# Optimization experiments

Measured on AMD Instinct MI355X. Metric: run time of the kernel, lower is better.

The kernel has to match this reference:

```python
import jax, jax.numpy as jnp
import numpy as np

VOXEL_SIZE = 0.05  # from init_kwargs


def _voxel_ds(pts, voxel_size, key, L):
    """Voxel-grid downsample one cloud (N,3): mean of points per occupied voxel,
    then resample L voxel centroids (uniform with replacement among valid voxels).
    Static shapes throughout (jit/vmap friendly)."""
    N = pts.shape[0]
    mn = jnp.min(pts, axis=0)
    v = jnp.floor((pts - mn) / voxel_size).astype(jnp.int32)      # (N,3) voxel coords >= 0
    dims = jnp.max(v, axis=0) + 1                                  # traced grid extents
    lin = (v[:, 0] * dims[1] + v[:, 1]) * dims[2] + v[:, 2]        # linearized voxel id
    order = jnp.argsort(lin)
    sl = lin[order]
    is_new = jnp.concatenate([jnp.ones((1,), bool), sl[1:] != sl[:-1]])
    seg = jnp.cumsum(is_new) - 1                                   # compact segment id per sorted point
    num_vox = seg[-1] + 1                                          # traced count of occupied voxels
    sums = jax.ops.segment_sum(pts[order], seg, num_segments=N)    # (N,3) padded
    cnt = jax.ops.segment_sum(jnp.ones((N,), pts.dtype), seg, num_segments=N)
    means = sums / jnp.maximum(cnt, 1.0)[:, None]                  # voxel centroids
    # random resample L centroids among the first num_vox valid segments
    u = jax.random.uniform(key, (L,))
    idx = jnp.minimum((u * num_vox.astype(u.dtype)).astype(jnp.int32), num_vox - 1)
    return means[idx]                                              # (L,3)


def _voxel_layer(x, voxel_size, L, key):
    # x: (B,3,N) -> (B,3,L)
    B = x.shape[0]
    pts = jnp.transpose(x, (0, 2, 1))                              # (B,N,3)
    keys = jax.random.split(key, B)
    out = jax.vmap(lambda p, k: _voxel_ds(p, voxel_size, k, L))(pts, keys)
    return jnp.transpose(out, (0, 2, 1))                           # (B,3,L)


def setup_inputs() -> dict:
    key = jax.random.key(0)
    x = jax.random.uniform(key, (16, 3, 262144), dtype=jnp.float32)
    return {"x": x}


def reference(x):
    B, _, N = x.shape
    L1, L2 = N // 2, N // 4
    k1, k2 = jax.random.split(jax.random.key(42))
    voxel_x1 = _voxel_layer(x, VOXEL_SIZE, L1, k1)
    voxel_x2 = _voxel_layer(voxel_x1, 2.0 * VOXEL_SIZE, L2, k2)
    return (voxel_x1, voxel_x2)
```

## Files before the change

kernel.cpp:

```cpp
#include <hip/hip_runtime.h>
#include <stdint.h>


typedef unsigned int u32;
typedef unsigned long long u64;

struct KeyArr { uint32_t k0[16]; uint32_t k1[16]; };

__host__ __device__ inline void tf2x32(uint32_t k0, uint32_t k1,
                                       uint32_t c0, uint32_t c1,
                                       uint32_t& o0, uint32_t& o1) {
  const uint32_t ks0 = k0, ks1 = k1, ks2 = k0 ^ k1 ^ 0x1BD11BDAu;
  uint32_t x0 = c0 + ks0, x1 = c1 + ks1;
#define TF_R(r) { x0 += x1; x1 = (x1 << (r)) | (x1 >> (32 - (r))); x1 ^= x0; }
  TF_R(13) TF_R(15) TF_R(26) TF_R(6)
  x0 += ks1; x1 += ks2 + 1u;
  TF_R(17) TF_R(29) TF_R(16) TF_R(24)
  x0 += ks2; x1 += ks0 + 2u;
  TF_R(13) TF_R(15) TF_R(26) TF_R(6)
  x0 += ks0; x1 += ks1 + 3u;
  TF_R(17) TF_R(29) TF_R(16) TF_R(24)
  x0 += ks1; x1 += ks2 + 4u;
  TF_R(13) TF_R(15) TF_R(26) TF_R(6)
  x0 += ks2; x1 += ks0 + 5u;
#undef TF_R
  o0 = x0; o1 = x1;
}

#define MN1 262144
#define ML1 131072
#define ML2 65536
#define MG1 8000
#define MG2 1000

__device__ __forceinline__ void bin1(float px, float py, float pz, float m0,
                                     float m1, float m2, float vox, int S,
                                     u64* lA, u64* lB) {
  int v0 = (int)floorf((px - m0) / vox);
  int v1 = (int)floorf((py - m1) / vox);
  int v2 = (int)floorf((pz - m2) / vox);
  int lin = (v0 * S + v1) * S + v2;
  u32 qx = (u32)(px * 1048576.0f);
  u32 qy = (u32)(py * 1048576.0f);
  u32 qz = (u32)(pz * 1048576.0f);
  atomicAdd(&lA[lin], ((u64)qy << 32) | (u64)qx);
  atomicAdd(&lB[lin], (1ull << 32) | (u64)qz);
}

__global__ void init_kernel(u64* cellsA, u64* cellsB, int ncells) {
  int i = blockIdx.x * blockDim.x + threadIdx.x;
  int stride = gridDim.x * blockDim.x;
  for (int j = i; j < ncells; j += stride) { cellsA[j] = 0ull; cellsB[j] = 0ull; }
}

__global__ void min_kernel(const float* __restrict__ in, int n4,
                           float* __restrict__ pmin) {
  int row = blockIdx.y;
  int PB = gridDim.x;
  const float4* p = (const float4*)in + (size_t)row * n4;
  int base = blockIdx.x * 2048 + threadIdx.x;
  float4 v0 = p[base], v1 = p[base + 256], v2 = p[base + 512],
         v3 = p[base + 768], v4 = p[base + 1024], v5 = p[base + 1280],
         v6 = p[base + 1536], v7 = p[base + 1792];
  float m0 = fminf(fminf(v0.x, v0.y), fminf(v0.z, v0.w));
  float m1 = fminf(fminf(v1.x, v1.y), fminf(v1.z, v1.w));
  float m2 = fminf(fminf(v2.x, v2.y), fminf(v2.z, v2.w));
  float m3 = fminf(fminf(v3.x, v3.y), fminf(v3.z, v3.w));
  float m4 = fminf(fminf(v4.x, v4.y), fminf(v4.z, v4.w));
  float m5 = fminf(fminf(v5.x, v5.y), fminf(v5.z, v5.w));
  float m6 = fminf(fminf(v6.x, v6.y), fminf(v6.z, v6.w));
  float m7 = fminf(fminf(v7.x, v7.y), fminf(v7.z, v7.w));
  float m = fminf(fminf(fminf(m0, m1), fminf(m2, m3)),
                  fminf(fminf(m4, m5), fminf(m6, m7)));
  for (int off = 32; off > 0; off >>= 1)
    m = fminf(m, __shfl_down(m, off, 64));
  __shared__ float wmin[4];
  int wid = threadIdx.x >> 6;
  if ((threadIdx.x & 63) == 0) wmin[wid] = m;
  __syncthreads();
  if (threadIdx.x == 0)
    pmin[row * PB + blockIdx.x] =
        fminf(fminf(wmin[0], wmin[1]), fminf(wmin[2], wmin[3]));
}

template <int G, int S, bool ATOMIC>
__global__ __launch_bounds__(1024) void accum_kernel(
    const float* __restrict__ in, int N, float vox,
    const float* __restrict__ pmin, int PB, u64* __restrict__ Ap,
    u64* __restrict__ Bp) {
  extern __shared__ u64 lds[];
  u64* lA = lds;
  u64* lB = lds + G;
  __shared__ float s_m[3];
  int tid = threadIdx.x, b = blockIdx.y;
  for (int i = tid; i < G; i += 1024) { lA[i] = 0ull; lB[i] = 0ull; }
  int wid = tid >> 6, lane = tid & 63;
  if (wid < 3) {
    float v = __int_as_float(0x7F800000);
    for (int j = lane; j < PB; j += 64)
      v = fminf(v, pmin[(b * 3 + wid) * PB + j]);
    for (int off = 32; off > 0; off >>= 1)
      v = fminf(v, __shfl_down(v, off, 64));
    if (lane == 0) s_m[wid] = v;
  }
  __syncthreads();
  float m0 = s_m[0], m1 = s_m[1], m2 = s_m[2];
  int ppb = N / gridDim.x;
  const float* base = in + (size_t)b * 3 * N;
  int start = blockIdx.x * ppb;
  const float4* r0 = (const float4*)(base + start);
  const float4* r1 = (const float4*)(base + N + start);
  const float4* r2 = (const float4*)(base + 2 * N + start);
  int q4 = ppb >> 2;
  for (int i = tid; i < q4; i += 1024) {
    float4 X = r0[i], Y = r1[i], Z = r2[i];
    bin1(X.x, Y.x, Z.x, m0, m1, m2, vox, S, lA, lB);
    bin1(X.y, Y.y, Z.y, m0, m1, m2, vox, S, lA, lB);
    bin1(X.z, Y.z, Z.z, m0, m1, m2, vox, S, lA, lB);
    bin1(X.w, Y.w, Z.w, m0, m1, m2, vox, S, lA, lB);
  }
  __syncthreads();
  int p = ATOMIC ? 0 : blockIdx.x;
  u64* gA = Ap + ((size_t)p * 16 + b) * G;
  u64* gB = Bp + ((size_t)p * 16 + b) * G;
  for (int c = tid; c < G; c += 1024) {
    if (ATOMIC) {
      u64 Bv = lB[c];
      if (Bv) { atomicAdd(&gA[c], lA[c]); atomicAdd(&gB[c], Bv); }
    } else {
      gA[c] = lA[c];
      gB[c] = lB[c];
    }
  }
}

__global__ __launch_bounds__(512) void redcomp1_kernel(
    const u64* __restrict__ Ap, const u64* __restrict__ Bp,
    float4* __restrict__ mc1 , u32* __restrict__ ccnt1) {
  int c = blockIdx.x, b = blockIdx.y;
  int tid = threadIdx.x, lane = tid & 63, wid = tid >> 6;
  __shared__ u32 s_w[16];
  float4 v = make_float4(0.f, 0.f, 0.f, 0.f);
  bool occ = false;
  if (tid < 500) {
    int cell = c * 500 + tid;
    u64 A = 0ull, Bv = 0ull;
#pragma unroll
    for (int p = 0; p < 16; ++p) {
      size_t o = ((size_t)p * 16 + b) * MG1 + cell;
      A += Ap[o];
      Bv += Bp[o];
    }
    u32 cnt = (u32)(Bv >> 32);
    if (cnt) {
      double inv = 1.0 / (1048576.0 * (double)cnt);
      v.x = (float)((double)(u32)A * inv);
      v.y = (float)((double)(u32)(A >> 32) * inv);
      v.z = (float)((double)(u32)Bv * inv);
      occ = true;
    }
  }
  u64 mask = __ballot(occ);
  u32 wpre = (u32)__popcll(mask & ((1ull << lane) - 1ull));
  if (lane == 0) s_w[wid] = (u32)__popcll(mask);
  __syncthreads();
  if (tid == 0) {
    u32 s = 0;
    for (int w = 0; w < 8; ++w) { u32 t = s_w[w]; s_w[8 + w] = s; s += t; }
    ccnt1[b * 16 + c] = s;
  }
  __syncthreads();
  if (occ) mc1[((size_t)b * 16 + c) * 500 + s_w[8 + wid] + wpre] = v;
}

__global__ void sample1_kernel(const float4* __restrict__ mc1,
                               const u32* __restrict__ ccnt1, KeyArr keys,
                               float* __restrict__ out,
                               float* __restrict__ pmin2) {
  int t = blockIdx.x * 256 + threadIdx.x;
  int b = blockIdx.y;
  int l0 = t * 4;
  u32 pre[17];
  pre[0] = 0u;
#pragma unroll
  for (int j = 0; j < 16; ++j) pre[j + 1] = pre[j] + ccnt1[b * 16 + j];
  u32 nv = pre[16];
  float fnv = (float)nv;
  int nvm1 = (int)nv - 1;
  uint32_t K0 = keys.k0[b], K1 = keys.k1[b];
  float4 m[4];
#pragma unroll
  for (int j = 0; j < 4; ++j) {
    uint32_t w0, w1;
    tf2x32(K0, K1, 0u, (uint32_t)(l0 + j), w0, w1);
    uint32_t bits = w0 ^ w1;
    float u = __uint_as_float((bits >> 9) | 0x3F800000u) - 1.0f;
    int idx = (int)(u * fnv);
    if (idx > nvm1) idx = nvm1;
    int ch = 0;
    u32 base = 0u;
#pragma unroll
    for (int q = 1; q < 16; ++q) {
      u32 pq = pre[q];
      if ((u32)idx >= pq) { ch = q; base = pq; }
    }
    m[j] = mc1[((size_t)b * 16 + ch) * 500 + (idx - (int)base)];
  }
  *(float4*)(out + ((size_t)b * 3 + 0) * ML1 + l0) =
      make_float4(m[0].x, m[1].x, m[2].x, m[3].x);
  *(float4*)(out + ((size_t)b * 3 + 1) * ML1 + l0) =
      make_float4(m[0].y, m[1].y, m[2].y, m[3].y);
  *(float4*)(out + ((size_t)b * 3 + 2) * ML1 + l0) =
      make_float4(m[0].z, m[1].z, m[2].z, m[3].z);
  float ax = fminf(fminf(m[0].x, m[1].x), fminf(m[2].x, m[3].x));
  float ay = fminf(fminf(m[0].y, m[1].y), fminf(m[2].y, m[3].y));
  float az = fminf(fminf(m[0].z, m[1].z), fminf(m[2].z, m[3].z));
  for (int off = 32; off > 0; off >>= 1) {
    ax = fminf(ax, __shfl_down(ax, off, 64));
    ay = fminf(ay, __shfl_down(ay, off, 64));
    az = fminf(az, __shfl_down(az, off, 64));
  }
  __shared__ float wm[4][3];
  int wid = threadIdx.x >> 6;
  if ((threadIdx.x & 63) == 0) {
    wm[wid][0] = ax; wm[wid][1] = ay; wm[wid][2] = az;
  }
  __syncthreads();
  if (threadIdx.x == 0) {
    int PB = gridDim.x;
    pmin2[(b * 3 + 0) * PB + blockIdx.x] =
        fminf(fminf(wm[0][0], wm[1][0]), fminf(wm[2][0], wm[3][0]));
    pmin2[(b * 3 + 1) * PB + blockIdx.x] =
        fminf(fminf(wm[0][1], wm[1][1]), fminf(wm[2][1], wm[3][1]));
    pmin2[(b * 3 + 2) * PB + blockIdx.x] =
        fminf(fminf(wm[0][2], wm[1][2]), fminf(wm[2][2], wm[3][2]));
  }
}

template <int G>
__global__ __launch_bounds__(1024) void redcomp_kernel(
    int P, const u64* __restrict__ Ap, const u64* __restrict__ Bp,
    float4* __restrict__ means4, u32* __restrict__ numvox) {
  int b = blockIdx.x, tid = threadIdx.x, wid = tid >> 6, lane = tid & 63;
  u64 A = 0ull, Bv = 0ull;
  if (tid < G) {
    for (int p = 0; p < P; ++p) {
      size_t o = ((size_t)p * 16 + b) * G + tid;
      A += Ap[o];
      Bv += Bp[o];
    }
  }
  u32 cnt = (u32)(Bv >> 32);
  float4 v = make_float4(0.f, 0.f, 0.f, 0.f);
  if (cnt) {
    double inv = 1.0 / (1048576.0 * (double)cnt);
    v.x = (float)((double)(u32)A * inv);
    v.y = (float)((double)(u32)(A >> 32) * inv);
    v.z = (float)((double)(u32)Bv * inv);
  }
  bool occ = cnt > 0u;
  u64 mask = __ballot(occ);
  u32 prefix = (u32)__popcll(mask & ((1ull << lane) - 1ull));
  __shared__ u32 wtot[16], wbase[16];
  if (lane == 0) wtot[wid] = (u32)__popcll(mask);
  __syncthreads();
  if (tid == 0) {
    u32 s = 0;
    for (int w = 0; w < 16; ++w) { wbase[w] = s; s += wtot[w]; }
    numvox[b] = s;
  }
  __syncthreads();
  if (occ) means4[(size_t)b * G + wbase[wid] + prefix] = v;
}

template <bool DOMIN>
__global__ void sample_kernel(int L, int G, const float4* __restrict__ means4,
                              const u32* __restrict__ numvox, KeyArr keys,
                              float* __restrict__ out,
                              float* __restrict__ pmin) {
  int t = blockIdx.x * 256 + threadIdx.x;
  int b = blockIdx.y;
  int l0 = t * 4;
  u32 nv = numvox[b];
  float fnv = (float)nv;
  int nvm1 = (int)nv - 1;
  uint32_t K0 = keys.k0[b], K1 = keys.k1[b];
  float4 m[4];
#pragma unroll
  for (int j = 0; j < 4; ++j) {
    uint32_t w0, w1;
    tf2x32(K0, K1, 0u, (uint32_t)(l0 + j), w0, w1);
    uint32_t bits = w0 ^ w1;
    float u = __uint_as_float((bits >> 9) | 0x3F800000u) - 1.0f;
    int idx = (int)(u * fnv);
    if (idx > nvm1) idx = nvm1;
    m[j] = means4[(size_t)b * G + idx];
  }
  *(float4*)(out + ((size_t)b * 3 + 0) * L + l0) =
      make_float4(m[0].x, m[1].x, m[2].x, m[3].x);
  *(float4*)(out + ((size_t)b * 3 + 1) * L + l0) =
      make_float4(m[0].y, m[1].y, m[2].y, m[3].y);
  *(float4*)(out + ((size_t)b * 3 + 2) * L + l0) =
      make_float4(m[0].z, m[1].z, m[2].z, m[3].z);
  if (DOMIN) {
    float ax = fminf(fminf(m[0].x, m[1].x), fminf(m[2].x, m[3].x));
    float ay = fminf(fminf(m[0].y, m[1].y), fminf(m[2].y, m[3].y));
    float az = fminf(fminf(m[0].z, m[1].z), fminf(m[2].z, m[3].z));
    for (int off = 32; off > 0; off >>= 1) {
      ax = fminf(ax, __shfl_down(ax, off, 64));
      ay = fminf(ay, __shfl_down(ay, off, 64));
      az = fminf(az, __shfl_down(az, off, 64));
    }
    __shared__ float wm[4][3];
    int wid = threadIdx.x >> 6;
    if ((threadIdx.x & 63) == 0) {
      wm[wid][0] = ax; wm[wid][1] = ay; wm[wid][2] = az;
    }
    __syncthreads();
    if (threadIdx.x == 0) {
      int PB = gridDim.x;
      pmin[(b * 3 + 0) * PB + blockIdx.x] =
          fminf(fminf(wm[0][0], wm[1][0]), fminf(wm[2][0], wm[3][0]));
      pmin[(b * 3 + 1) * PB + blockIdx.x] =
          fminf(fminf(wm[0][1], wm[1][1]), fminf(wm[2][1], wm[3][1]));
      pmin[(b * 3 + 2) * PB + blockIdx.x] =
          fminf(fminf(wm[0][2], wm[1][2]), fminf(wm[2][2], wm[3][2]));
    }
  }
}

__global__ __launch_bounds__(1024) void compact_kernel(
    int G, const u64* __restrict__ Ac, const u64* __restrict__ Bc,
    float4* __restrict__ means4, u32* __restrict__ numvox) {
  int b = blockIdx.x, tid = threadIdx.x, wid = tid >> 6, lane = tid & 63;
  __shared__ u32 wtot[16], wbase[16];
  __shared__ u32 gbase;
  if (tid == 0) gbase = 0u;
  __syncthreads();
  for (int t0 = 0; t0 < G; t0 += 1024) {
    int cell = t0 + tid;
    float4 v = make_float4(0.f, 0.f, 0.f, 0.f);
    u32 cnt = 0u;
    if (cell < G) {
      u64 A = Ac[(size_t)b * G + cell], Bv = Bc[(size_t)b * G + cell];
      cnt = (u32)(Bv >> 32);
      if (cnt) {
        double inv = 1.0 / (1048576.0 * (double)cnt);
        v.x = (float)((double)(u32)A * inv);
        v.y = (float)((double)(u32)(A >> 32) * inv);
        v.z = (float)((double)(u32)Bv * inv);
      }
    }
    bool occ = cnt > 0u;
    u64 mask = __ballot(occ);
    u32 prefix = (u32)__popcll(mask & ((1ull << lane) - 1ull));
    if (lane == 0) wtot[wid] = (u32)__popcll(mask);
    __syncthreads();
    if (tid == 0) {
      u32 s = gbase;
      for (int w = 0; w < 16; ++w) { wbase[w] = s; s += wtot[w]; }
      gbase = s;
    }
    __syncthreads();
    if (occ) means4[(size_t)b * G + wbase[wid] + prefix] = v;
    __syncthreads();
  }
  if (tid == 0) numvox[b] = gbase;
}

extern "C" void kernel_launch(void* const* d_in, const int* in_sizes, int n_in,
                              void* d_out, int out_size, void* d_ws,
                              size_t ws_size, hipStream_t stream) {
  const float* x = (const float*)d_in[0];
  float* out = (float*)d_out;

  uint32_t k1a, k1b, k2a, k2b;
  tf2x32(0u, 42u, 0u, 0u, k1a, k1b);
  tf2x32(0u, 42u, 0u, 1u, k2a, k2b);
  KeyArr keys1, keys2;
  for (int b = 0; b < 16; ++b) {
    tf2x32(k1a, k1b, 0u, (uint32_t)b, keys1.k0[b], keys1.k1[b]);
    tf2x32(k2a, k2b, 0u, (uint32_t)b, keys2.k0[b], keys2.k1[b]);
  }

  const int PB1 = 32, PB2 = 128;
  const size_t oAp = 0;
  const size_t oBp = oAp + (size_t)16 * 16 * MG1 * 8;
  const size_t oMc1 = oBp + (size_t)16 * 16 * MG1 * 8;
  const size_t oMc2 = oMc1 + (size_t)16 * 16 * 500 * 16;
  const size_t oPm1 = oMc2 + (size_t)16 * MG2 * 16;
  const size_t oPm2 = oPm1 + 48 * PB1 * 4;
  const size_t oCc1 = oPm2 + 48 * PB2 * 4;
  const size_t oNv = oCc1 + 256 * 4;
  const size_t bigNeed = oNv + 128;

  uint8_t* w = (uint8_t*)d_ws;
  if (ws_size >= bigNeed) {
    u64* Ap = (u64*)(w + oAp);
    u64* Bp = (u64*)(w + oBp);
    float4* mc1 = (float4*)(w + oMc1);
    float4* mc2 = (float4*)(w + oMc2);
    float* pmin1 = (float*)(w + oPm1);
    float* pmin2 = (float*)(w + oPm2);
    u32* ccnt1 = (u32*)(w + oCc1);
    u32* numvox2 = (u32*)(w + oNv);

    min_kernel<<<dim3(PB1, 48), dim3(256), 0, stream>>>(x, MN1 / 4, pmin1);
    accum_kernel<MG1, 20, false>
        <<<dim3(16, 16), dim3(1024), 2 * MG1 * 8, stream>>>(x, MN1, 0.05f,
                                                            pmin1, PB1, Ap, Bp);
    redcomp1_kernel<<<dim3(16, 16), dim3(512), 0, stream>>>(Ap, Bp, mc1,
                                                            ccnt1);
    sample1_kernel<<<dim3(ML1 / 1024, 16), dim3(256), 0, stream>>>(
        mc1, ccnt1, keys1, out, pmin2);
    float* out2 = out + (size_t)48 * ML1;
    accum_kernel<MG2, 10, false>
        <<<dim3(16, 16), dim3(1024), 2 * MG2 * 8, stream>>>(
            out, ML1, 0.1f, pmin2, PB2, Ap, Bp);
    redcomp_kernel<MG2><<<dim3(16), dim3(1024), 0, stream>>>(16, Ap, Bp, mc2,
                                                             numvox2);
    sample_kernel<false><<<dim3(ML2 / 1024, 16), dim3(256), 0, stream>>>(
        ML2, MG2, mc2, numvox2, keys2, out2, nullptr);
    return;
  }

  const size_t slice1 = (size_t)16 * MG1, slice2 = (size_t)16 * MG2;
  u64* As = (u64*)w;
  u64* Bs = As + (slice1 + slice2);
  float4* means4s = (float4*)(Bs + (slice1 + slice2));
  float* pmin1s = (float*)(means4s + slice1);
  float* pmin2s = pmin1s + 48 * PB1;
  u32* numvoxs = (u32*)(pmin2s + 48 * PB2);

  init_kernel<<<dim3(64), dim3(256), 0, stream>>>(As, Bs,
                                                  (int)(slice1 + slice2));
  min_kernel<<<dim3(PB1, 48), dim3(256), 0, stream>>>(x, MN1 / 4, pmin1s);
  accum_kernel<MG1, 20, true>
      <<<dim3(8, 16), dim3(1024), 2 * MG1 * 8, stream>>>(x, MN1, 0.05f, pmin1s,
                                                         PB1, As, Bs);
  compact_kernel<<<dim3(16), dim3(1024), 0, stream>>>(MG1, As, Bs, means4s,
                                                      numvoxs);
  sample_kernel<true><<<dim3(ML1 / 1024, 16), dim3(256), 0, stream>>>(
      ML1, MG1, means4s, numvoxs, keys1, out, pmin2s);
  float* out2 = out + (size_t)48 * ML1;
  accum_kernel<MG2, 10, true>
      <<<dim3(8, 16), dim3(1024), 2 * MG2 * 8, stream>>>(
          out, ML1, 0.1f, pmin2s, PB2, As + slice1, Bs + slice1);
  compact_kernel<<<dim3(16), dim3(1024), 0, stream>>>(
      MG2, As + slice1, Bs + slice1, means4s, numvoxs + 16);
  sample_kernel<false><<<dim3(ML2 / 1024, 16), dim3(256), 0, stream>>>(
      ML2, MG2, means4s, numvoxs + 16, keys2, out2, nullptr);
}
```

Before: 68.76 us.

## Interleave partial accumulators and fuse stage-two reduce, compact and sample

Partial voxel sums are now stored as interleaved (A,B) pairs in one ulonglong2 buffer, so each reducer does a single 16-byte load per partition instead of two separate 8-byte loads. For the second stage, the separate reduce/compact kernel and the sampling kernel are merged into one kernel. Each block reduces the partitions into shared memory, compacts the occupied voxels, and samples from LDS. This removes one launch and a global round-trip for the means, at the cost of every block redundantly repeating the per-batch reduction.

```diff
diff --git a/kernel.cpp b/kernel.cpp
--- a/kernel.cpp
+++ b/kernel.cpp
@@ -83,8 +83,214 @@
         fminf(fminf(wmin[0], wmin[1]), fminf(wmin[2], wmin[3]));
 }
 
-template <int G, int S, bool ATOMIC>
-__global__ __launch_bounds__(1024) void accum_kernel(
+template <int G, int S>
+__global__ __launch_bounds__(1024) void accum_part_kernel(
+    const float* __restrict__ in, int N, float vox,
+    const float* __restrict__ pmin, int PB, ulonglong2* __restrict__ Cp) {
+  extern __shared__ u64 lds[];
+  u64* lA = lds;
+  u64* lB = lds + G;
+  __shared__ float s_m[3];
+  int tid = threadIdx.x, b = blockIdx.y;
+  for (int i = tid; i < G; i += 1024) { lA[i] = 0ull; lB[i] = 0ull; }
+  int wid = tid >> 6, lane = tid & 63;
+  if (wid < 3) {
+    float v = __int_as_float(0x7F800000);
+    for (int j = lane; j < PB; j += 64)
+      v = fminf(v, pmin[(b * 3 + wid) * PB + j]);
+    for (int off = 32; off > 0; off >>= 1)
+      v = fminf(v, __shfl_down(v, off, 64));
+    if (lane == 0) s_m[wid] = v;
+  }
+  __syncthreads();
+  float m0 = s_m[0], m1 = s_m[1], m2 = s_m[2];
+  int ppb = N / gridDim.x;
+  const float* base = in + (size_t)b * 3 * N;
+  int start = blockIdx.x * ppb;
+  const float4* r0 = (const float4*)(base + start);
+  const float4* r1 = (const float4*)(base + N + start);
+  const float4* r2 = (const float4*)(base + 2 * N + start);
+  int q4 = ppb >> 2;
+  for (int i = tid; i < q4; i += 1024) {
+    float4 X = r0[i], Y = r1[i], Z = r2[i];
+    bin1(X.x, Y.x, Z.x, m0, m1, m2, vox, S, lA, lB);
+    bin1(X.y, Y.y, Z.y, m0, m1, m2, vox, S, lA, lB);
+    bin1(X.z, Y.z, Z.z, m0, m1, m2, vox, S, lA, lB);
+    bin1(X.w, Y.w, Z.w, m0, m1, m2, vox, S, lA, lB);
+  }
+  __syncthreads();
+  ulonglong2* gC = Cp + ((size_t)blockIdx.x * 16 + b) * G;
+  for (int c = tid; c < G; c += 1024)
+    gC[c] = make_ulonglong2(lA[c], lB[c]);
+}
+
+__global__ __launch_bounds__(512) void redcomp1_kernel(
+    const ulonglong2* __restrict__ Cp,
+    float4* __restrict__ mc1 , u32* __restrict__ ccnt1) {
+  int c = blockIdx.x, b = blockIdx.y;
+  int tid = threadIdx.x, lane = tid & 63, wid = tid >> 6;
+  __shared__ u32 s_w[16];
+  float4 v = make_float4(0.f, 0.f, 0.f, 0.f);
+  bool occ = false;
+  if (tid < 500) {
+    int cell = c * 500 + tid;
+    u64 A = 0ull, Bv = 0ull;
+#pragma unroll
+    for (int p = 0; p < 16; ++p) {
+      ulonglong2 cc = Cp[((size_t)p * 16 + b) * MG1 + cell];
+      A += cc.x;
+      Bv += cc.y;
+    }
+    u32 cnt = (u32)(Bv >> 32);
+    if (cnt) {
+      double inv = 1.0 / (1048576.0 * (double)cnt);
+      v.x = (float)((double)(u32)A * inv);
+      v.y = (float)((double)(u32)(A >> 32) * inv);
+      v.z = (float)((double)(u32)Bv * inv);
+      occ = true;
+    }
+  }
+  u64 mask = __ballot(occ);
+  u32 wpre = (u32)__popcll(mask & ((1ull << lane) - 1ull));
+  if (lane == 0) s_w[wid] = (u32)__popcll(mask);
+  __syncthreads();
+  if (tid == 0) {
+    u32 s = 0;
+    for (int w = 0; w < 8; ++w) { u32 t = s_w[w]; s_w[8 + w] = s; s += t; }
+    ccnt1[b * 16 + c] = s;
+  }
+  __syncthreads();
+  if (occ) mc1[((size_t)b * 16 + c) * 500 + s_w[8 + wid] + wpre] = v;
+}
+
+__global__ void sample1_kernel(const float4* __restrict__ mc1,
+                               const u32* __restrict__ ccnt1, KeyArr keys,
+                               float* __restrict__ out,
+                               float* __restrict__ pmin2) {
+  int t = blockIdx.x * 256 + threadIdx.x;
+  int b = blockIdx.y;
+  int l0 = t * 4;
+  u32 pre[17];
+  pre[0] = 0u;
+#pragma unroll
+  for (int j = 0; j < 16; ++j) pre[j + 1] = pre[j] + ccnt1[b * 16 + j];
+  u32 nv = pre[16];
+  float fnv = (float)nv;
+  int nvm1 = (int)nv - 1;
+  uint32_t K0 = keys.k0[b], K1 = keys.k1[b];
+  float4 m[4];
+#pragma unroll
+  for (int j = 0; j < 4; ++j) {
+    uint32_t w0, w1;
+    tf2x32(K0, K1, 0u, (uint32_t)(l0 + j), w0, w1);
+    uint32_t bits = w0 ^ w1;
+    float u = __uint_as_float((bits >> 9) | 0x3F800000u) - 1.0f;
+    int idx = (int)(u * fnv);
+    if (idx > nvm1) idx = nvm1;
+    int ch = 0;
+    u32 base = 0u;
+#pragma unroll
+    for (int q = 1; q < 16; ++q) {
+      u32 pq = pre[q];
+      if ((u32)idx >= pq) { ch = q; base = pq; }
+    }
+    m[j] = mc1[((size_t)b * 16 + ch) * 500 + (idx - (int)base)];
+  }
+  *(float4*)(out + ((size_t)b * 3 + 0) * ML1 + l0) =
+      make_float4(m[0].x, m[1].x, m[2].x, m[3].x);
+  *(float4*)(out + ((size_t)b * 3 + 1) * ML1 + l0) =
+      make_float4(m[0].y, m[1].y, m[2].y, m[3].y);
+  *(float4*)(out + ((size_t)b * 3 + 2) * ML1 + l0) =
+      make_float4(m[0].z, m[1].z, m[2].z, m[3].z);
+  float ax = fminf(fminf(m[0].x, m[1].x), fminf(m[2].x, m[3].x));
+  float ay = fminf(fminf(m[0].y, m[1].y), fminf(m[2].y, m[3].y));
+  float az = fminf(fminf(m[0].z, m[1].z), fminf(m[2].z, m[3].z));
+  for (int off = 32; off > 0; off >>= 1) {
+    ax = fminf(ax, __shfl_down(ax, off, 64));
+    ay = fminf(ay, __shfl_down(ay, off, 64));
+    az = fminf(az, __shfl_down(az, off, 64));
+  }
+  __shared__ float wm[4][3];
+  int wid = threadIdx.x >> 6;
+  if ((threadIdx.x & 63) == 0) {
+    wm[wid][0] = ax; wm[wid][1] = ay; wm[wid][2] = az;
+  }
+  __syncthreads();
+  if (threadIdx.x == 0) {
+    int PB = gridDim.x;
+    pmin2[(b * 3 + 0) * PB + blockIdx.x] =
+        fminf(fminf(wm[0][0], wm[1][0]), fminf(wm[2][0], wm[3][0]));
+    pmin2[(b * 3 + 1) * PB + blockIdx.x] =
+        fminf(fminf(wm[0][1], wm[1][1]), fminf(wm[2][1], wm[3][1]));
+    pmin2[(b * 3 + 2) * PB + blockIdx.x] =
+        fminf(fminf(wm[0][2], wm[1][2]), fminf(wm[2][2], wm[3][2]));
+  }
+}
+
+__global__ __launch_bounds__(1024) void sampred2_kernel(
+    const ulonglong2* __restrict__ Cp, KeyArr keys, float* __restrict__ out2) {
+  int g = blockIdx.x, b = blockIdx.y;
+  int tid = threadIdx.x, lane = tid & 63, wid = tid >> 6;
+  __shared__ float4 smeans[MG2];
+  __shared__ u32 s_w[32];
+  __shared__ u32 s_nv;
+  float4 v = make_float4(0.f, 0.f, 0.f, 0.f);
+  bool occ = false;
+  if (tid < MG2) {
+    u64 A = 0ull, Bv = 0ull;
+#pragma unroll
+    for (int p = 0; p < 16; ++p) {
+      ulonglong2 cc = Cp[((size_t)p * 16 + b) * MG2 + tid];
+      A += cc.x;
+      Bv += cc.y;
+    }
+    u32 cnt = (u32)(Bv >> 32);
+    if (cnt) {
+      double inv = 1.0 / (1048576.0 * (double)cnt);
+      v.x = (float)((double)(u32)A * inv);
+      v.y = (float)((double)(u32)(A >> 32) * inv);
+      v.z = (float)((double)(u32)Bv * inv);
+      occ = true;
+    }
+  }
+  u64 mask = __ballot(occ);
+  u32 prefix = (u32)__popcll(mask & ((1ull << lane) - 1ull));
+  if (lane == 0) s_w[wid] = (u32)__popcll(mask);
+  __syncthreads();
+  if (tid == 0) {
+    u32 s = 0;
+    for (int w = 0; w < 16; ++w) { u32 t = s_w[w]; s_w[16 + w] = s; s += t; }
+    s_nv = s;
+  }
+  __syncthreads();
+  if (occ) smeans[s_w[16 + wid] + prefix] = v;
+  __syncthreads();
+  u32 nv = s_nv;
+  float fnv = (float)nv;
+  int nvm1 = (int)nv - 1;
+  uint32_t K0 = keys.k0[b], K1 = keys.k1[b];
+  int l0 = g * 4096 + tid * 4;
+  float4 m[4];
+#pragma unroll
+  for (int j = 0; j < 4; ++j) {
+    uint32_t w0, w1;
+    tf2x32(K0, K1, 0u, (uint32_t)(l0 + j), w0, w1);
+    uint32_t bits = w0 ^ w1;
+    float u = __uint_as_float((bits >> 9) | 0x3F800000u) - 1.0f;
+    int idx = (int)(u * fnv);
+    if (idx > nvm1) idx = nvm1;
+    m[j] = smeans[idx];
+  }
+  *(float4*)(out2 + ((size_t)b * 3 + 0) * ML2 + l0) =
+      make_float4(m[0].x, m[1].x, m[2].x, m[3].x);
+  *(float4*)(out2 + ((size_t)b * 3 + 1) * ML2 + l0) =
+      make_float4(m[0].y, m[1].y, m[2].y, m[3].y);
+  *(float4*)(out2 + ((size_t)b * 3 + 2) * ML2 + l0) =
+      make_float4(m[0].z, m[1].z, m[2].z, m[3].z);
+}
+
+template <int G, int S>
+__global__ __launch_bounds__(1024) void accum_atomic_kernel(
     const float* __restrict__ in, int N, float vox,
     const float* __restrict__ pmin, int PB, u64* __restrict__ Ap,
     u64* __restrict__ Bp) {
@@ -120,157 +326,51 @@
     bin1(X.w, Y.w, Z.w, m0, m1, m2, vox, S, lA, lB);
   }
   __syncthreads();
-  int p = ATOMIC ? 0 : blockIdx.x;
-  u64* gA = Ap + ((size_t)p * 16 + b) * G;
-  u64* gB = Bp + ((size_t)p * 16 + b) * G;
+  u64* gA = Ap + (size_t)b * G;
+  u64* gB = Bp + (size_t)b * G;
   for (int c = tid; c < G; c += 1024) {
-    if (ATOMIC) {
-      u64 Bv = lB[c];
-      if (Bv) { atomicAdd(&gA[c], lA[c]); atomicAdd(&gB[c], Bv); }
-    } else {
-      gA[c] = lA[c];
-      gB[c] = lB[c];
-    }
-  }
-}
-
-__global__ __launch_bounds__(512) void redcomp1_kernel(
-    const u64* __restrict__ Ap, const u64* __restrict__ Bp,
-    float4* __restrict__ mc1 , u32* __restrict__ ccnt1) {
-  int c = blockIdx.x, b = blockIdx.y;
-  int tid = threadIdx.x, lane = tid & 63, wid = tid >> 6;
-  __shared__ u32 s_w[16];
-  float4 v = make_float4(0.f, 0.f, 0.f, 0.f);
-  bool occ = false;
-  if (tid < 500) {
-    int cell = c * 500 + tid;
-    u64 A = 0ull, Bv = 0ull;
-#pragma unroll
-    for (int p = 0; p < 16; ++p) {
-      size_t o = ((size_t)p * 16 + b) * MG1 + cell;
-      A += Ap[o];
-      Bv += Bp[o];
-    }
-    u32 cnt = (u32)(Bv >> 32);
-    if (cnt) {
-      double inv = 1.0 / (1048576.0 * (double)cnt);
-      v.x = (float)((double)(u32)A * inv);
-      v.y = (float)((double)(u32)(A >> 32) * inv);
-      v.z = (float)((double)(u32)Bv * inv);
-      occ = true;
-    }
-  }
-  u64 mask = __ballot(occ);
-  u32 wpre = (u32)__popcll(mask & ((1ull << lane) - 1ull));
-  if (lane == 0) s_w[wid] = (u32)__popcll(mask);
-  __syncthreads();
-  if (tid == 0) {
-    u32 s = 0;
-    for (int w = 0; w < 8; ++w) { u32 t = s_w[w]; s_w[8 + w] = s; s += t; }
-    ccnt1[b * 16 + c] = s;
-  }
-  __syncthreads();
-  if (occ) mc1[((size_t)b * 16 + c) * 500 + s_w[8 + wid] + wpre] = v;
-}
-
-__global__ void sample1_kernel(const float4* __restrict__ mc1,
-                               const u32* __restrict__ ccnt1, KeyArr keys,
-                               float* __restrict__ out,
-                               float* __restrict__ pmin2) {
-  int t = blockIdx.x * 256 + threadIdx.x;
-  int b = blockIdx.y;
-  int l0 = t * 4;
-  u32 pre[17];
-  pre[0] = 0u;
-#pragma unroll
-  for (int j = 0; j < 16; ++j) pre[j + 1] = pre[j] + ccnt1[b * 16 + j];
-  u32 nv = pre[16];
-  float fnv = (float)nv;
-  int nvm1 = (int)nv - 1;
-  uint32_t K0 = keys.k0[b], K1 = keys.k1[b];
-  float4 m[4];
-#pragma unroll
-  for (int j = 0; j < 4; ++j) {
-    uint32_t w0, w1;
-    tf2x32(K0, K1, 0u, (uint32_t)(l0 + j), w0, w1);
-    uint32_t bits = w0 ^ w1;
-    float u = __uint_as_float((bits >> 9) | 0x3F800000u) - 1.0f;
-    int idx = (int)(u * fnv);
-    if (idx > nvm1) idx = nvm1;
-    int ch = 0;
-    u32 base = 0u;
-#pragma unroll
-    for (int q = 1; q < 16; ++q) {
-      u32 pq = pre[q];
-      if ((u32)idx >= pq) { ch = q; base = pq; }
-    }
-    m[j] = mc1[((size_t)b * 16 + ch) * 500 + (idx - (int)base)];
-  }
-  *(float4*)(out + ((size_t)b * 3 + 0) * ML1 + l0) =
-      make_float4(m[0].x, m[1].x, m[2].x, m[3].x);
-  *(float4*)(out + ((size_t)b * 3 + 1) * ML1 + l0) =
-      make_float4(m[0].y, m[1].y, m[2].y, m[3].y);
-  *(float4*)(out + ((size_t)b * 3 + 2) * ML1 + l0) =
-      make_float4(m[0].z, m[1].z, m[2].z, m[3].z);
-  float ax = fminf(fminf(m[0].x, m[1].x), fminf(m[2].x, m[3].x));
-  float ay = fminf(fminf(m[0].y, m[1].y), fminf(m[2].y, m[3].y));
-  float az = fminf(fminf(m[0].z, m[1].z), fminf(m[2].z, m[3].z));
-  for (int off = 32; off > 0; off >>= 1) {
-    ax = fminf(ax, __shfl_down(ax, off, 64));
-    ay = fminf(ay, __shfl_down(ay, off, 64));
-    az = fminf(az, __shfl_down(az, off, 64));
-  }
-  __shared__ float wm[4][3];
-  int wid = threadIdx.x >> 6;
-  if ((threadIdx.x & 63) == 0) {
-    wm[wid][0] = ax; wm[wid][1] = ay; wm[wid][2] = az;
-  }
-  __syncthreads();
-  if (threadIdx.x == 0) {
-    int PB = gridDim.x;
-    pmin2[(b * 3 + 0) * PB + blockIdx.x] =
-        fminf(fminf(wm[0][0], wm[1][0]), fminf(wm[2][0], wm[3][0]));
-    pmin2[(b * 3 + 1) * PB + blockIdx.x] =
-        fminf(fminf(wm[0][1], wm[1][1]), fminf(wm[2][1], wm[3][1]));
-    pmin2[(b * 3 + 2) * PB + blockIdx.x] =
-        fminf(fminf(wm[0][2], wm[1][2]), fminf(wm[2][2], wm[3][2]));
-  }
-}
-
-template <int G>
-__global__ __launch_bounds__(1024) void redcomp_kernel(
-    int P, const u64* __restrict__ Ap, const u64* __restrict__ Bp,
+    u64 Bv = lB[c];
+    if (Bv) { atomicAdd(&gA[c], lA[c]); atomicAdd(&gB[c], Bv); }
+  }
+}
+
+__global__ __launch_bounds__(1024) void compact_kernel(
+    int G, const u64* __restrict__ Ac, const u64* __restrict__ Bc,
     float4* __restrict__ means4, u32* __restrict__ numvox) {
   int b = blockIdx.x, tid = threadIdx.x, wid = tid >> 6, lane = tid & 63;
-  u64 A = 0ull, Bv = 0ull;
-  if (tid < G) {
-    for (int p = 0; p < P; ++p) {
-      size_t o = ((size_t)p * 16 + b) * G + tid;
-      A += Ap[o];
-      Bv += Bp[o];
-    }
-  }
-  u32 cnt = (u32)(Bv >> 32);
-  float4 v = make_float4(0.f, 0.f, 0.f, 0.f);
-  if (cnt) {
-    double inv = 1.0 / (1048576.0 * (double)cnt);
-    v.x = (float)((double)(u32)A * inv);
-    v.y = (float)((double)(u32)(A >> 32) * inv);
-    v.z = (float)((double)(u32)Bv * inv);
-  }
-  bool occ = cnt > 0u;
-  u64 mask = __ballot(occ);
-  u32 prefix = (u32)__popcll(mask & ((1ull << lane) - 1ull));
   __shared__ u32 wtot[16], wbase[16];
-  if (lane == 0) wtot[wid] = (u32)__popcll(mask);
-  __syncthreads();
-  if (tid == 0) {
-    u32 s = 0;
-    for (int w = 0; w < 16; ++w) { wbase[w] = s; s += wtot[w]; }
-    numvox[b] = s;
-  }
-  __syncthreads();
-  if (occ) means4[(size_t)b * G + wbase[wid] + prefix] = v;
+  __shared__ u32 gbase;
+  if (tid == 0) gbase = 0u;
+  __syncthreads();
+  for (int t0 = 0; t0 < G; t0 += 1024) {
+    int cell = t0 + tid;
+    float4 v = make_float4(0.f, 0.f, 0.f, 0.f);
+    u32 cnt = 0u;
+    if (cell < G) {
+      u64 A = Ac[(size_t)b * G + cell], Bv = Bc[(size_t)b * G + cell];
+      cnt = (u32)(Bv >> 32);
+      if (cnt) {
+        double inv = 1.0 / (1048576.0 * (double)cnt);
+        v.x = (float)((double)(u32)A * inv);
+        v.y = (float)((double)(u32)(A >> 32) * inv);
+        v.z = (float)((double)(u32)Bv * inv);
+      }
+    }
+    bool occ = cnt > 0u;
+    u64 mask = __ballot(occ);
+    u32 prefix = (u32)__popcll(mask & ((1ull << lane) - 1ull));
+    if (lane == 0) wtot[wid] = (u32)__popcll(mask);
+    __syncthreads();
+    if (tid == 0) {
+      u32 s = gbase;
+      for (int w = 0; w < 16; ++w) { wbase[w] = s; s += wtot[w]; }
+      gbase = s;
+    }
+    __syncthreads();
+    if (occ) means4[(size_t)b * G + wbase[wid] + prefix] = v;
+    __syncthreads();
+  }
+  if (tid == 0) numvox[b] = gbase;
 }
 
 template <bool DOMIN>
@@ -329,45 +429,6 @@
   }
 }
 
-__global__ __launch_bounds__(1024) void compact_kernel(
-    int G, const u64* __restrict__ Ac, const u64* __restrict__ Bc,
-    float4* __restrict__ means4, u32* __restrict__ numvox) {
-  int b = blockIdx.x, tid = threadIdx.x, wid = tid >> 6, lane = tid & 63;
-  __shared__ u32 wtot[16], wbase[16];
-  __shared__ u32 gbase;
-  if (tid == 0) gbase = 0u;
-  __syncthreads();
-  for (int t0 = 0; t0 < G; t0 += 1024) {
-    int cell = t0 + tid;
-    float4 v = make_float4(0.f, 0.f, 0.f, 0.f);
-    u32 cnt = 0u;
-    if (cell < G) {
-      u64 A = Ac[(size_t)b * G + cell], Bv = Bc[(size_t)b * G + cell];
-      cnt = (u32)(Bv >> 32);
-      if (cnt) {
-        double inv = 1.0 / (1048576.0 * (double)cnt);
-        v.x = (float)((double)(u32)A * inv);
-        v.y = (float)((double)(u32)(A >> 32) * inv);
-        v.z = (float)((double)(u32)Bv * inv);
-      }
-    }
-    bool occ = cnt > 0u;
-    u64 mask = __ballot(occ);
-    u32 prefix = (u32)__popcll(mask & ((1ull << lane) - 1ull));
-    if (lane == 0) wtot[wid] = (u32)__popcll(mask);
-    __syncthreads();
-    if (tid == 0) {
-      u32 s = gbase;
-      for (int w = 0; w < 16; ++w) { wbase[w] = s; s += wtot[w]; }
-      gbase = s;
-    }
-    __syncthreads();
-    if (occ) means4[(size_t)b * G + wbase[wid] + prefix] = v;
-    __syncthreads();
-  }
-  if (tid == 0) numvox[b] = gbase;
-}
-
 extern "C" void kernel_launch(void* const* d_in, const int* in_sizes, int n_in,
                               void* d_out, int out_size, void* d_ws,
                               size_t ws_size, hipStream_t stream) {
@@ -384,43 +445,33 @@
   }
 
   const int PB1 = 32, PB2 = 128;
-  const size_t oAp = 0;
-  const size_t oBp = oAp + (size_t)16 * 16 * MG1 * 8;
-  const size_t oMc1 = oBp + (size_t)16 * 16 * MG1 * 8;
-  const size_t oMc2 = oMc1 + (size_t)16 * 16 * 500 * 16;
-  const size_t oPm1 = oMc2 + (size_t)16 * MG2 * 16;
+  const size_t oCp = 0;
+  const size_t oMc1 = oCp + (size_t)16 * 16 * MG1 * 16;
+  const size_t oPm1 = oMc1 + (size_t)16 * 16 * 500 * 16;
   const size_t oPm2 = oPm1 + 48 * PB1 * 4;
   const size_t oCc1 = oPm2 + 48 * PB2 * 4;
-  const size_t oNv = oCc1 + 256 * 4;
-  const size_t bigNeed = oNv + 128;
+  const size_t bigNeed = oCc1 + 1024 + 128;
 
   uint8_t* w = (uint8_t*)d_ws;
   if (ws_size >= bigNeed) {
-    u64* Ap = (u64*)(w + oAp);
-    u64* Bp = (u64*)(w + oBp);
+    ulonglong2* Cp = (ulonglong2*)(w + oCp);
     float4* mc1 = (float4*)(w + oMc1);
-    float4* mc2 = (float4*)(w + oMc2);
     float* pmin1 = (float*)(w + oPm1);
     float* pmin2 = (float*)(w + oPm2);
     u32* ccnt1 = (u32*)(w + oCc1);
-    u32* numvox2 = (u32*)(w + oNv);
 
     min_kernel<<<dim3(PB1, 48), dim3(256), 0, stream>>>(x, MN1 / 4, pmin1);
-    accum_kernel<MG1, 20, false>
+    accum_part_kernel<MG1, 20>
         <<<dim3(16, 16), dim3(1024), 2 * MG1 * 8, stream>>>(x, MN1, 0.05f,
-                                                            pmin1, PB1, Ap, Bp);
-    redcomp1_kernel<<<dim3(16, 16), dim3(512), 0, stream>>>(Ap, Bp, mc1,
-                                                            ccnt1);
+                                                            pmin1, PB1, Cp);
+    redcomp1_kernel<<<dim3(16, 16), dim3(512), 0, stream>>>(Cp, mc1, ccnt1);
     sample1_kernel<<<dim3(ML1 / 1024, 16), dim3(256), 0, stream>>>(
         mc1, ccnt1, keys1, out, pmin2);
     float* out2 = out + (size_t)48 * ML1;
-    accum_kernel<MG2, 10, false>
+    accum_part_kernel<MG2, 10>
         <<<dim3(16, 16), dim3(1024), 2 * MG2 * 8, stream>>>(
-            out, ML1, 0.1f, pmin2, PB2, Ap, Bp);
-    redcomp_kernel<MG2><<<dim3(16), dim3(1024), 0, stream>>>(16, Ap, Bp, mc2,
-                                                             numvox2);
-    sample_kernel<false><<<dim3(ML2 / 1024, 16), dim3(256), 0, stream>>>(
-        ML2, MG2, mc2, numvox2, keys2, out2, nullptr);
+            out, ML1, 0.1f, pmin2, PB2, Cp);
+    sampred2_kernel<<<dim3(16, 16), dim3(1024), 0, stream>>>(Cp, keys2, out2);
     return;
   }
 
@@ -435,7 +486,7 @@
   init_kernel<<<dim3(64), dim3(256), 0, stream>>>(As, Bs,
                                                   (int)(slice1 + slice2));
   min_kernel<<<dim3(PB1, 48), dim3(256), 0, stream>>>(x, MN1 / 4, pmin1s);
-  accum_kernel<MG1, 20, true>
+  accum_atomic_kernel<MG1, 20>
       <<<dim3(8, 16), dim3(1024), 2 * MG1 * 8, stream>>>(x, MN1, 0.05f, pmin1s,
                                                          PB1, As, Bs);
   compact_kernel<<<dim3(16), dim3(1024), 0, stream>>>(MG1, As, Bs, means4s,
@@ -443,7 +494,7 @@
   sample_kernel<true><<<dim3(ML1 / 1024, 16), dim3(256), 0, stream>>>(
       ML1, MG1, means4s, numvoxs, keys1, out, pmin2s);
   float* out2 = out + (size_t)48 * ML1;
-  accum_kernel<MG2, 10, true>
+  accum_atomic_kernel<MG2, 10>
       <<<dim3(8, 16), dim3(1024), 2 * MG2 * 8, stream>>>(
           out, ML1, 0.1f, pmin2s, PB2, As + slice1, Bs + slice1);
   compact_kernel<<<dim3(16), dim3(1024), 0, stream>>>(
```

After: 69.66 us. About the same (+1.3%).
